# Performance work log

Hardware: AMD Instinct MI355X
Metric: run time of the kernel (lower is better)

Reference implementation:

```python
import jax, jax.numpy as jnp
import numpy as np

EMBED = 1024

def setup_inputs() -> dict:
    key = jax.random.key(0)
    ks = jax.random.split(key, 10)
    B, S, E = 4, 2048, EMBED
    inv = 1.0 / np.sqrt(E)
    return {
        "query": jax.random.normal(ks[0], (B, S, E), jnp.float32),
        "key": jax.random.normal(ks[1], (B, S, E), jnp.float32),
        "value": jax.random.normal(ks[2], (B, S, E), jnp.float32),
        "attn_mask": jnp.zeros((B, S, S), jnp.float32),
        "Wq": jax.random.normal(ks[3], (E, E), jnp.float32) * inv,
        "bq": jnp.zeros((E,), jnp.float32),
        "Wk": jax.random.normal(ks[4], (E, E), jnp.float32) * inv,
        "bk": jnp.zeros((E,), jnp.float32),
        "Wv": jax.random.normal(ks[5], (E, E), jnp.float32) * inv,
        "bv": jnp.zeros((E,), jnp.float32),
    }

def reference(query, key, value, attn_mask, Wq, bq, Wk, bk, Wv, bv):
    E = query.shape[-1]
    q = query @ Wq.T + bq            # [B,S,E]
    k = key @ Wk.T + bk              # [B,S,E]
    v = value @ Wv.T + bv            # [B,S,E]
    scores = jnp.einsum('bse,bte->bst', q, k) / jnp.sqrt(jnp.float32(E))
    scores = scores + attn_mask      # [B,S,S]
    attn = jax.nn.softmax(scores, axis=-1)
    return jnp.einsum('bst,bte->bse', attn, v)
```

## Files before the change

### kernel.cpp

```cpp
#include <hip/hip_runtime.h>
#include <cstdint>
#include <cstddef>

typedef __bf16 bf16;
typedef __bf16 bf16x8 __attribute__((ext_vector_type(8)));
typedef float  f32x4  __attribute__((ext_vector_type(4)));

#define NB 4
#define SS 2048
#define EE 1024

#define BUFB  24576
#define LDS3  (3 * BUFB)
#define LDS6  (6 * BUFB)

static __device__ __forceinline__ void glds16(const bf16* g, void* l)
{
    __builtin_amdgcn_global_load_lds(
        (const __attribute__((address_space(1))) unsigned int*)g,
        (__attribute__((address_space(3))) unsigned int*)l,
        16, 0, 0);
}

static __device__ __forceinline__ void swz_block(int& bx, int& by, int& bz)
{
    const int nx = gridDim.x, ny = gridDim.y;
    const int nwg = nx * ny * gridDim.z;
    int lin = blockIdx.x + nx * (blockIdx.y + ny * blockIdx.z);
    const int per = nwg >> 3;
    lin = (lin & 7) * per + (lin >> 3);
    bz = lin / (nx * ny);
    const int r = lin - bz * nx * ny;
    by = r / nx;
    bx = r - by * nx;
}

template<int NBUF>
static __device__ __forceinline__ void kloop32(
    const bf16* __restrict__ A, const bf16* __restrict__ Bm,
    int lda, int ldb, int nt, char* lds, int m0, int n0, int tid,
    f32x4 acc[4][4])
{
    const int lane = tid & 63, w = tid >> 6;
    const int wm = w >> 2, wn = w & 3;
    const int lr = lane & 15, kq = lane >> 4;
    const int cb = (kq * 16) ^ ((lr & 3) << 4);

    const int srow   = tid >> 2;
    const int chunkL = (tid & 3) ^ (srow & 3);
    const bf16* Asrc = A  + (size_t)(m0 + srow) * lda + chunkL * 8;
    const bf16* Bsrc = Bm + (size_t)(n0 + srow) * ldb + chunkL * 8;
    const int wofs = w << 10;

#pragma unroll
    for (int p = 0; p < NBUF - 1; ++p) {
        char* d = lds + p * BUFB + wofs;
        const int kt = p * 32;
        glds16(Asrc + kt,                     d);
        glds16(Bsrc + kt,                     d + 8192);
        glds16(Bsrc + (size_t)128 * ldb + kt, d + 16384);
    }
    if constexpr (NBUF == 3) asm volatile("s_waitcnt vmcnt(3)" ::: "memory");
    else                     asm volatile("s_waitcnt vmcnt(12)" ::: "memory");
    __builtin_amdgcn_sched_barrier(0);
    __builtin_amdgcn_s_barrier();
    __builtin_amdgcn_sched_barrier(0);

    int rb = 0, sb = NBUF - 1;
    for (int t = 0; t < nt; ++t) {
        char* la = lds + rb * BUFB;
        char* lb = la + 8192;
        const int ts = (t + NBUF - 1 < nt) ? t + NBUF - 1 : nt - 1;
        const int kt = ts * 32;
        char* d = lds + sb * BUFB + wofs;

        bf16x8 af[4], bg[4];
#pragma unroll
        for (int m = 0; m < 4; ++m)
            af[m] = *(const bf16x8*)(la + (wm * 64 + m * 16 + lr) * 64 + cb);
#pragma unroll
        for (int n = 0; n < 4; ++n)
            bg[n] = *(const bf16x8*)(lb + (wn * 64 + n * 16 + lr) * 64 + cb);

        glds16(Asrc + kt,                     d);
        glds16(Bsrc + kt,                     d + 8192);
        glds16(Bsrc + (size_t)128 * ldb + kt, d + 16384);

        __builtin_amdgcn_s_setprio(1);
#pragma unroll
        for (int m = 0; m < 4; ++m)
#pragma unroll
            for (int n = 0; n < 4; ++n)
                acc[m][n] = __builtin_amdgcn_mfma_f32_16x16x32_bf16(af[m], bg[n], acc[m][n], 0, 0, 0);
        __builtin_amdgcn_s_setprio(0);

        if (t < nt - 1) {
            if constexpr (NBUF == 3) asm volatile("s_waitcnt vmcnt(3)" ::: "memory");
            else                     asm volatile("s_waitcnt vmcnt(12)" ::: "memory");
            __builtin_amdgcn_sched_barrier(0);
            __builtin_amdgcn_s_barrier();
            __builtin_amdgcn_sched_barrier(0);
        }
        rb = (rb + 1 == NBUF) ? 0 : rb + 1;
        sb = (sb + 1 == NBUF) ? 0 : sb + 1;
    }
    asm volatile("s_waitcnt vmcnt(0)" ::: "memory");
}

__global__ __launch_bounds__(256) void cvt3_kernel(
    const float* __restrict__ s0, const float* __restrict__ s1, const float* __restrict__ s2,
    bf16* __restrict__ d0, bf16* __restrict__ d1, bf16* __restrict__ d2, unsigned n)
{
    const float* s; bf16* d;
    if (blockIdx.y == 0)      { s = s0; d = d0; }
    else if (blockIdx.y == 1) { s = s1; d = d1; }
    else                      { s = s2; d = d2; }
    const size_t i = ((size_t)blockIdx.x * 256 + threadIdx.x) * 8;
    if (i >= n) return;
    const float4 f0 = *(const float4*)(s + i);
    const float4 f1 = *(const float4*)(s + i + 4);
    bf16x8 h;
    h[0] = (bf16)f0.x; h[1] = (bf16)f0.y; h[2] = (bf16)f0.z; h[3] = (bf16)f0.w;
    h[4] = (bf16)f1.x; h[5] = (bf16)f1.y; h[6] = (bf16)f1.z; h[7] = (bf16)f1.w;
    *(bf16x8*)(d + i) = h;
}

__global__ __launch_bounds__(512, 4) void proj8(
    const bf16* __restrict__ qc, const bf16* __restrict__ kc, const bf16* __restrict__ vc,
    const bf16* __restrict__ Wc,
    const float* __restrict__ bq, const float* __restrict__ bk, const float* __restrict__ bv,
    bf16* __restrict__ qb, bf16* __restrict__ kb, bf16* __restrict__ vb)
{
    extern __shared__ char lds[];
    int bx, by, bz; swz_block(bx, by, bz);
    const bf16* A; const float* bias; bf16* out;
    if (bz == 0)      { A = qc; bias = bq; out = qb; }
    else if (bz == 1) { A = kc; bias = bk; out = kb; }
    else              { A = vc; bias = bv; out = vb; }
    const bf16* Bm = Wc + (size_t)bz * EE * EE;

    const int m0 = by * 128, n0 = bx * 256;
    const int tid = threadIdx.x;

    f32x4 acc[4][4];
#pragma unroll
    for (int m = 0; m < 4; ++m)
#pragma unroll
        for (int n = 0; n < 4; ++n) { acc[m][n][0] = 0.f; acc[m][n][1] = 0.f; acc[m][n][2] = 0.f; acc[m][n][3] = 0.f; }

    kloop32<3>(A, Bm, EE, EE, EE / 32, lds, m0, n0, tid, acc);

    const int lane = tid & 63, w = tid >> 6, wm = w >> 2, wn = w & 3;
    const int lr = lane & 15, kq = lane >> 4;
#pragma unroll
    for (int n = 0; n < 4; ++n) {
        const int gcol = n0 + wn * 64 + n * 16 + lr;
        const float bb = bias[gcol];
#pragma unroll
        for (int m = 0; m < 4; ++m)
#pragma unroll
            for (int j = 0; j < 4; ++j) {
                const int grow = m0 + wm * 64 + m * 16 + kq * 4 + j;
                out[(size_t)grow * EE + gcol] = (bf16)(acc[m][n][j] + bb);
            }
    }
}

__global__ __launch_bounds__(256) void transpose_kernel(const bf16* __restrict__ vb,
                                                        bf16* __restrict__ vt)
{
    __shared__ bf16 t[64][72];
    const int b  = blockIdx.z;
    const int s0 = blockIdx.x * 64, e0 = blockIdx.y * 64;
    const int tid = threadIdx.x;

    const bf16* src = vb + ((size_t)b * SS + s0) * EE + e0;
#pragma unroll
    for (int i = 0; i < 2; ++i) {
        const int c  = tid * 2 + i;
        const int r  = c >> 3;
        const int cc = (c & 7) * 8;
        *(uint4*)&t[r][cc] = *(const uint4*)&src[(size_t)r * EE + cc];
    }
    __syncthreads();

    bf16* dst = vt + ((size_t)b * EE + e0) * SS + s0;
    const int er  = tid >> 2;
    const int sc0 = (tid & 3) * 16;
    bf16 tmp[16];
#pragma unroll
    for (int k2 = 0; k2 < 16; ++k2) tmp[k2] = t[sc0 + k2][er];
    *(uint4*)&dst[(size_t)er * SS + sc0]     = *(uint4*)&tmp[0];
    *(uint4*)&dst[(size_t)er * SS + sc0 + 8] = *(uint4*)&tmp[8];
}

__global__ __launch_bounds__(512, 4) void scores8(const bf16* __restrict__ qb,
                                                  const bf16* __restrict__ kb,
                                                  const float* __restrict__ mask,
                                                  bf16* __restrict__ sc)
{
    extern __shared__ char lds[];
    int bx, by, bz; swz_block(bx, by, bz);
    const bf16* A  = qb + (size_t)bz * SS * EE;
    const bf16* Bm = kb + (size_t)bz * SS * EE;

    const int m0 = by * 128, n0 = bx * 256;
    const int tid = threadIdx.x;

    f32x4 acc[4][4];
#pragma unroll
    for (int m = 0; m < 4; ++m)
#pragma unroll
        for (int n = 0; n < 4; ++n) { acc[m][n][0] = 0.f; acc[m][n][1] = 0.f; acc[m][n][2] = 0.f; acc[m][n][3] = 0.f; }

    kloop32<3>(A, Bm, EE, EE, EE / 32, lds, m0, n0, tid, acc);

    const int lane = tid & 63, w = tid >> 6, wm = w >> 2, wn = w & 3;
    const int lr = lane & 15, kq = lane >> 4;
    const float* mrow = mask + (size_t)bz * SS * SS;
    bf16* out = sc + (size_t)bz * SS * SS;
    const float scale = 0.03125f;
#pragma unroll
    for (int m = 0; m < 4; ++m)
#pragma unroll
        for (int n = 0; n < 4; ++n)
#pragma unroll
            for (int j = 0; j < 4; ++j) {
                const int grow = m0 + wm * 64 + m * 16 + kq * 4 + j;
                const int gcol = n0 + wn * 64 + n * 16 + lr;
                const float v = acc[m][n][j] * scale + mrow[(size_t)grow * SS + gcol];
                out[(size_t)grow * SS + gcol] = (bf16)v;
            }
}

__global__ __launch_bounds__(256) void softmax_kernel(bf16* __restrict__ sc)
{
    __shared__ float red[4];
    const size_t row = blockIdx.x;
    uint4* rp = (uint4*)(sc + row * (size_t)SS);
    const int tid = threadIdx.x, lane = tid & 63, wid = tid >> 6;

    const uint4 d = rp[tid];
    const unsigned int u[4] = { d.x, d.y, d.z, d.w };
    float f[8];
#pragma unroll
    for (int i = 0; i < 4; ++i) {
        union { unsigned int i_; float f_; } lo, hi;
        lo.i_ = u[i] << 16;
        hi.i_ = u[i] & 0xffff0000u;
        f[2 * i]     = lo.f_;
        f[2 * i + 1] = hi.f_;
    }

    float m = f[0];
#pragma unroll
    for (int i = 1; i < 8; ++i) m = fmaxf(m, f[i]);
#pragma unroll
    for (int o = 32; o > 0; o >>= 1) m = fmaxf(m, __shfl_xor(m, o));
    if (lane == 0) red[wid] = m;
    __syncthreads();
    m = fmaxf(fmaxf(red[0], red[1]), fmaxf(red[2], red[3]));
    __syncthreads();

    float e[8], s = 0.f;
#pragma unroll
    for (int i = 0; i < 8; ++i) { e[i] = __expf(f[i] - m); s += e[i]; }
#pragma unroll
    for (int o = 32; o > 0; o >>= 1) s += __shfl_xor(s, o);
    if (lane == 0) red[wid] = s;
    __syncthreads();
    s = red[0] + red[1] + red[2] + red[3];
    const float inv = 1.0f / s;

    unsigned int ou[4];
#pragma unroll
    for (int i = 0; i < 4; ++i) {
        union { bf16 h; unsigned short b; } a0, a1;
        a0.h = (bf16)(e[2 * i] * inv);
        a1.h = (bf16)(e[2 * i + 1] * inv);
        ou[i] = ((unsigned int)a1.b << 16) | (unsigned int)a0.b;
    }
    rp[tid] = make_uint4(ou[0], ou[1], ou[2], ou[3]);
}

__global__ __launch_bounds__(512, 2) void pv8(const bf16* __restrict__ sc,
                                              const bf16* __restrict__ vt,
                                              float* __restrict__ outp)
{
    extern __shared__ char lds[];
    int bx, by, bz; swz_block(bx, by, bz);
    const bf16* A  = sc + (size_t)bz * SS * SS;
    const bf16* Bm = vt + (size_t)bz * EE * SS;

    const int m0 = by * 128, n0 = bx * 256;
    const int tid = threadIdx.x;

    f32x4 acc[4][4];
#pragma unroll
    for (int m = 0; m < 4; ++m)
#pragma unroll
        for (int n = 0; n < 4; ++n) { acc[m][n][0] = 0.f; acc[m][n][1] = 0.f; acc[m][n][2] = 0.f; acc[m][n][3] = 0.f; }

    kloop32<6>(A, Bm, SS, SS, SS / 32, lds, m0, n0, tid, acc);

    const int lane = tid & 63, w = tid >> 6, wm = w >> 2, wn = w & 3;
    const int lr = lane & 15, kq = lane >> 4;
#pragma unroll
    for (int m = 0; m < 4; ++m)
#pragma unroll
        for (int n = 0; n < 4; ++n)
#pragma unroll
            for (int j = 0; j < 4; ++j) {
                const int grow = m0 + wm * 64 + m * 16 + kq * 4 + j;
                const int gcol = n0 + wn * 64 + n * 16 + lr;
                outp[((size_t)bz * SS + grow) * EE + gcol] = acc[m][n][j];
            }
}

extern "C" void kernel_launch(void* const* d_in, const int* in_sizes, int n_in,
                              void* d_out, int out_size, void* d_ws, size_t ws_size,
                              hipStream_t stream)
{
    const float* query = (const float*)d_in[0];
    const float* key_  = (const float*)d_in[1];
    const float* value = (const float*)d_in[2];
    const float* mask  = (const float*)d_in[3];
    const float* Wq = (const float*)d_in[4];
    const float* bq = (const float*)d_in[5];
    const float* Wk = (const float*)d_in[6];
    const float* bk = (const float*)d_in[7];
    const float* Wv = (const float*)d_in[8];
    const float* bv = (const float*)d_in[9];
    float* outp = (float*)d_out;

    char* ws = (char*)d_ws;
    const size_t QKV = (size_t)NB * SS * EE * 2;
    const size_t SCB = (size_t)NB * SS * SS * 2;
    const size_t WCB = (size_t)3 * EE * EE * 2;
    if (ws_size < 4 * QKV + SCB + WCB) return;

    bf16* qb = (bf16*)(ws);
    bf16* kb = (bf16*)(ws + QKV);
    bf16* vb = (bf16*)(ws + 2 * QKV);
    bf16* vt = (bf16*)(ws + 3 * QKV);
    bf16* sc = (bf16*)(ws + 4 * QKV);
    bf16* Wc = (bf16*)(ws + 4 * QKV + SCB);
    bf16* qc = vt;
    bf16* kc = sc;
    bf16* vc = (bf16*)(ws + 5 * QKV);

    (void)hipFuncSetAttribute((const void*)proj8,   hipFuncAttributeMaxDynamicSharedMemorySize, LDS3);
    (void)hipFuncSetAttribute((const void*)scores8, hipFuncAttributeMaxDynamicSharedMemorySize, LDS3);
    (void)hipFuncSetAttribute((const void*)pv8,     hipFuncAttributeMaxDynamicSharedMemorySize, LDS6);

    dim3 blk(256), blk5(512);
    const unsigned NQKV = (unsigned)NB * SS * EE;
    const unsigned NW   = (unsigned)EE * EE;
    cvt3_kernel<<<dim3(NQKV / (256 * 8), 3), blk, 0, stream>>>(
        query, key_, value, qc, kc, vc, NQKV);
    cvt3_kernel<<<dim3(NW / (256 * 8), 3), blk, 0, stream>>>(
        Wq, Wk, Wv, Wc, Wc + (size_t)EE * EE, Wc + 2 * (size_t)EE * EE, NW);

    proj8<<<dim3(EE / 256, (NB * SS) / 128, 3), blk5, LDS3, stream>>>(
        qc, kc, vc, Wc, bq, bk, bv, qb, kb, vb);
    transpose_kernel<<<dim3(SS / 64, EE / 64, NB), blk, 0, stream>>>(vb, vt);
    scores8<<<dim3(SS / 256, SS / 128, NB), blk5, LDS3, stream>>>(qb, kb, mask, sc);
    softmax_kernel<<<dim3(NB * SS), blk, 0, stream>>>(sc);
    pv8<<<dim3(EE / 256, SS / 128, NB), blk5, LDS6, stream>>>(sc, vt, outp);
}
```

Before: 203.6 us.

## Change LDS swizzle, use triple buffering in PV, merge conversion launches

```diff
diff --git a/kernel.cpp b/kernel.cpp
--- a/kernel.cpp
+++ b/kernel.cpp
@@ -12,7 +12,6 @@
 
 #define BUFB  24576
 #define LDS3  (3 * BUFB)
-#define LDS6  (6 * BUFB)
 
 static __device__ __forceinline__ void glds16(const bf16* g, void* l)
 {
@@ -35,19 +34,19 @@
     bx = r - by * nx;
 }
 
-template<int NBUF>
 static __device__ __forceinline__ void kloop32(
     const bf16* __restrict__ A, const bf16* __restrict__ Bm,
     int lda, int ldb, int nt, char* lds, int m0, int n0, int tid,
     f32x4 acc[4][4])
 {
+    constexpr int NBUF = 3;
     const int lane = tid & 63, w = tid >> 6;
     const int wm = w >> 2, wn = w & 3;
     const int lr = lane & 15, kq = lane >> 4;
-    const int cb = (kq * 16) ^ ((lr & 3) << 4);
+    const int cb = ((kq ^ ((lr >> 1) & 3)) << 4);
 
     const int srow   = tid >> 2;
-    const int chunkL = (tid & 3) ^ (srow & 3);
+    const int chunkL = (tid & 3) ^ ((srow >> 1) & 3);
     const bf16* Asrc = A  + (size_t)(m0 + srow) * lda + chunkL * 8;
     const bf16* Bsrc = Bm + (size_t)(n0 + srow) * ldb + chunkL * 8;
     const int wofs = w << 10;
@@ -60,8 +59,7 @@
         glds16(Bsrc + kt,                     d + 8192);
         glds16(Bsrc + (size_t)128 * ldb + kt, d + 16384);
     }
-    if constexpr (NBUF == 3) asm volatile("s_waitcnt vmcnt(3)" ::: "memory");
-    else                     asm volatile("s_waitcnt vmcnt(12)" ::: "memory");
+    asm volatile("s_waitcnt vmcnt(3)" ::: "memory");
     __builtin_amdgcn_sched_barrier(0);
     __builtin_amdgcn_s_barrier();
     __builtin_amdgcn_sched_barrier(0);
@@ -95,8 +93,7 @@
         __builtin_amdgcn_s_setprio(0);
 
         if (t < nt - 1) {
-            if constexpr (NBUF == 3) asm volatile("s_waitcnt vmcnt(3)" ::: "memory");
-            else                     asm volatile("s_waitcnt vmcnt(12)" ::: "memory");
+            asm volatile("s_waitcnt vmcnt(3)" ::: "memory");
             __builtin_amdgcn_sched_barrier(0);
             __builtin_amdgcn_s_barrier();
             __builtin_amdgcn_sched_barrier(0);
@@ -107,16 +104,23 @@
     asm volatile("s_waitcnt vmcnt(0)" ::: "memory");
 }
 
-__global__ __launch_bounds__(256) void cvt3_kernel(
-    const float* __restrict__ s0, const float* __restrict__ s1, const float* __restrict__ s2,
-    bf16* __restrict__ d0, bf16* __restrict__ d1, bf16* __restrict__ d2, unsigned n)
-{
-    const float* s; bf16* d;
-    if (blockIdx.y == 0)      { s = s0; d = d0; }
-    else if (blockIdx.y == 1) { s = s1; d = d1; }
-    else                      { s = s2; d = d2; }
-    const size_t i = ((size_t)blockIdx.x * 256 + threadIdx.x) * 8;
-    if (i >= n) return;
+__global__ __launch_bounds__(256) void cvt_all(
+    const float* __restrict__ q, const float* __restrict__ k, const float* __restrict__ v,
+    const float* __restrict__ Wq, const float* __restrict__ Wk, const float* __restrict__ Wv,
+    bf16* __restrict__ qc, bf16* __restrict__ kc, bf16* __restrict__ vc,
+    bf16* __restrict__ Wc)
+{
+    const int y = blockIdx.y;
+    const float* s; bf16* d; size_t i;
+    if (blockIdx.x < 4096) {
+        s = (y == 0) ? q : (y == 1) ? k : v;
+        d = (y == 0) ? qc : (y == 1) ? kc : vc;
+        i = ((size_t)blockIdx.x * 256 + threadIdx.x) * 8;
+    } else {
+        s = (y == 0) ? Wq : (y == 1) ? Wk : Wv;
+        d = Wc + (size_t)y * EE * EE;
+        i = ((size_t)(blockIdx.x - 4096) * 256 + threadIdx.x) * 8;
+    }
     const float4 f0 = *(const float4*)(s + i);
     const float4 f1 = *(const float4*)(s + i + 4);
     bf16x8 h;
@@ -148,7 +152,7 @@
 #pragma unroll
         for (int n = 0; n < 4; ++n) { acc[m][n][0] = 0.f; acc[m][n][1] = 0.f; acc[m][n][2] = 0.f; acc[m][n][3] = 0.f; }
 
-    kloop32<3>(A, Bm, EE, EE, EE / 32, lds, m0, n0, tid, acc);
+    kloop32(A, Bm, EE, EE, EE / 32, lds, m0, n0, tid, acc);
 
     const int lane = tid & 63, w = tid >> 6, wm = w >> 2, wn = w & 3;
     const int lr = lane & 15, kq = lane >> 4;
@@ -213,7 +217,7 @@
 #pragma unroll
         for (int n = 0; n < 4; ++n) { acc[m][n][0] = 0.f; acc[m][n][1] = 0.f; acc[m][n][2] = 0.f; acc[m][n][3] = 0.f; }
 
-    kloop32<3>(A, Bm, EE, EE, EE / 32, lds, m0, n0, tid, acc);
+    kloop32(A, Bm, EE, EE, EE / 32, lds, m0, n0, tid, acc);
 
     const int lane = tid & 63, w = tid >> 6, wm = w >> 2, wn = w & 3;
     const int lr = lane & 15, kq = lane >> 4;
@@ -283,7 +287,7 @@
     rp[tid] = make_uint4(ou[0], ou[1], ou[2], ou[3]);
 }
 
-__global__ __launch_bounds__(512, 2) void pv8(const bf16* __restrict__ sc,
+__global__ __launch_bounds__(512, 4) void pv8(const bf16* __restrict__ sc,
                                               const bf16* __restrict__ vt,
                                               float* __restrict__ outp)
 {
@@ -301,7 +305,7 @@
 #pragma unroll
         for (int n = 0; n < 4; ++n) { acc[m][n][0] = 0.f; acc[m][n][1] = 0.f; acc[m][n][2] = 0.f; acc[m][n][3] = 0.f; }
 
-    kloop32<6>(A, Bm, SS, SS, SS / 32, lds, m0, n0, tid, acc);
+    kloop32(A, Bm, SS, SS, SS / 32, lds, m0, n0, tid, acc);
 
     const int lane = tid & 63, w = tid >> 6, wm = w >> 2, wn = w & 3;
     const int lr = lane & 15, kq = lane >> 4;
@@ -351,20 +355,16 @@
 
     (void)hipFuncSetAttribute((const void*)proj8,   hipFuncAttributeMaxDynamicSharedMemorySize, LDS3);
     (void)hipFuncSetAttribute((const void*)scores8, hipFuncAttributeMaxDynamicSharedMemorySize, LDS3);
-    (void)hipFuncSetAttribute((const void*)pv8,     hipFuncAttributeMaxDynamicSharedMemorySize, LDS6);
+    (void)hipFuncSetAttribute((const void*)pv8,     hipFuncAttributeMaxDynamicSharedMemorySize, LDS3);
 
     dim3 blk(256), blk5(512);
-    const unsigned NQKV = (unsigned)NB * SS * EE;
-    const unsigned NW   = (unsigned)EE * EE;
-    cvt3_kernel<<<dim3(NQKV / (256 * 8), 3), blk, 0, stream>>>(
-        query, key_, value, qc, kc, vc, NQKV);
-    cvt3_kernel<<<dim3(NW / (256 * 8), 3), blk, 0, stream>>>(
-        Wq, Wk, Wv, Wc, Wc + (size_t)EE * EE, Wc + 2 * (size_t)EE * EE, NW);
+    cvt_all<<<dim3(4096 + 512, 3), blk, 0, stream>>>(
+        query, key_, value, Wq, Wk, Wv, qc, kc, vc, Wc);
 
     proj8<<<dim3(EE / 256, (NB * SS) / 128, 3), blk5, LDS3, stream>>>(
         qc, kc, vc, Wc, bq, bk, bv, qb, kb, vb);
     transpose_kernel<<<dim3(SS / 64, EE / 64, NB), blk, 0, stream>>>(vb, vt);
     scores8<<<dim3(SS / 256, SS / 128, NB), blk5, LDS3, stream>>>(qb, kb, mask, sc);
     softmax_kernel<<<dim3(NB * SS), blk, 0, stream>>>(sc);
-    pv8<<<dim3(EE / 256, SS / 128, NB), blk5, LDS6, stream>>>(sc, vt, outp);
-}
+    pv8<<<dim3(EE / 256, SS / 128, NB), blk5, LDS3, stream>>>(sc, vt, outp);
+}
```

Result: no change. 203.7 us (+0.1%).
